# Optimization experiments

Measured on AMD Instinct MI355X. Metric: run time of the kernel, lower is better.

Reference implementation:

```python
import jax, jax.numpy as jnp
import numpy as np

N_NODES = 100000
N_EDGES = 1600000
D_FEAT = 128
UNITS = 128
LEAKY_ALPHA = 0.2  # tf.nn.leaky_relu default


def setup_inputs() -> dict:
    key = jax.random.key(0)
    k1, k2, k3, k4 = jax.random.split(key, 4)
    node_states = jax.random.normal(k1, (N_NODES, D_FEAT), dtype=jnp.float32)
    edges = jax.random.randint(k2, (N_EDGES, 2), 0, N_NODES, dtype=jnp.int64)
    kernel = jax.random.normal(k3, (D_FEAT, UNITS), dtype=jnp.float32) * (1.0 / np.sqrt(D_FEAT))
    kernel_attention = jax.random.normal(k4, (2 * UNITS, 1), dtype=jnp.float32) * (1.0 / np.sqrt(2 * UNITS))
    return {
        "node_states": node_states,
        "edges": edges,
        "kernel": kernel,
        "kernel_attention": kernel_attention,
    }


def reference(node_states, edges, kernel, kernel_attention):
    n = node_states.shape[0]
    tgt_idx = edges[:, 0]
    src_idx = edges[:, 1]

    # node_states_transformed: [N, units]
    h = node_states @ kernel

    # Attention logits. concat([tgt, src]) @ ka == tgt @ ka_t + src @ ka_s
    # (avoids materializing the [E, 2*units] concat).
    ka_t = kernel_attention[:UNITS, 0]   # [units]
    ka_s = kernel_attention[UNITS:, 0]   # [units]
    score_t = h @ ka_t                   # [N]
    score_s = h @ ka_s                   # [N]
    e = score_t[tgt_idx] + score_s[src_idx]              # [E]
    e = jax.nn.leaky_relu(e, negative_slope=LEAKY_ALPHA)
    e = jnp.exp(jnp.clip(e, -2.0, 2.0))

    # Segment softmax over incoming edges of each target node.
    sum_e = jax.ops.segment_sum(e, tgt_idx, num_segments=n)  # [N]
    attention = e / (sum_e[tgt_idx] + 1e-9)                  # [E]

    # Weighted scatter-sum of source messages.
    messages = h[src_idx] * attention[:, None]               # [E, units]
    output = jax.ops.segment_sum(messages, tgt_idx, num_segments=n)  # [N, units]
    return output
```

## Files before the change

### kernel.cpp

```cpp
#include <hip/hip_runtime.h>
#include <stdint.h>

typedef unsigned short ushort_t;
typedef __attribute__((ext_vector_type(8))) short short8;
typedef __attribute__((ext_vector_type(4))) float float4v;
typedef __attribute__((ext_vector_type(2))) float float2v;

#define N_NODES 100000
#define N_EDGES 1600000
#define D 128
#define NB_GEMM 1563
#define NBG     521
#define NB_B1   250
#define EPB     6400
#define BUCKETS 782
#define CAP     2560

static __device__ __forceinline__ float2v up2(uint32_t u) {
    float2v r;
    r.x = __builtin_bit_cast(float, u << 16);
    r.y = __builtin_bit_cast(float, u & 0xffff0000u);
    return r;
}
static __device__ __forceinline__ uint32_t f2bf_u(float f) {
    uint32_t u = __builtin_bit_cast(uint32_t, f);
    return (u + 0x7fffu + ((u >> 16) & 1u)) >> 16;
}
static __device__ __forceinline__ ushort_t f2bf(float f) {
    return (ushort_t)f2bf_u(f);
}
static __device__ __forceinline__ uint32_t pack2(float a, float b) {
    return f2bf_u(a) | (f2bf_u(b) << 16);
}
static __device__ __forceinline__ float edge_e(float s) {
    float x = (s >= 0.0f) ? s : 0.2f * s;
    x = fminf(fmaxf(x, -2.0f), 2.0f);
    return __expf(x);
}

__global__ void __launch_bounds__(256) prep_kernel(const float* __restrict__ W,
                                                   const float* __restrict__ KA,
                                                   float* __restrict__ wa,
                                                   const int* __restrict__ E,
                                                   int* __restrict__ eflag) {
    __shared__ int s;
    int b = blockIdx.x, t = threadIdx.x;
    if (b == 0) {
        if (t == 0) s = 0;
        __syncthreads();
        int nz = 0;
#pragma unroll
        for (int j = 0; j < 8; j++)
            if (E[(t + j * 256) * 2 + 1] != 0) nz = 1;
        if (nz) atomicOr(&s, 1);
        __syncthreads();
        if (t == 0) *eflag = (s == 0) ? 1 : 0;
    } else {
        int half = t >> 7, k = t & 127;
        const float* kav = KA + half * 128;
        const float* wrow = W + k * 128;
        float acc = 0.0f;
#pragma unroll 8
        for (int j = 0; j < 128; j++) acc += wrow[j] * kav[j];
        wa[half * 128 + k] = acc;
    }
}

__global__ void __launch_bounds__(256) fused_kernel(const float* __restrict__ X,
                                                    const float* __restrict__ W,
                                                    const float* __restrict__ wa,
                                                    ushort_t* __restrict__ H,
                                                    float* __restrict__ st,
                                                    float* __restrict__ ss,
                                                    int M,
                                                    const int* __restrict__ E,
                                                    const int* __restrict__ eflag,
                                                    int* __restrict__ sortedE,
                                                    ushort_t* __restrict__ bmat,
                                                    ushort_t* __restrict__ lofs) {
    __shared__ __align__(16) ushort_t lds_raw[16384];
    int tid = threadIdx.x;
    if (blockIdx.x >= NBG) {
        int eb = blockIdx.x - NBG;
        int* lhist = (int*)lds_raw;
        int* lpart = ((int*)lds_raw) + 1024;
        int t = tid;
        for (int j = t; j < 1024; j += 256) lhist[j] = 0;
        __syncthreads();
        int i64 = *eflag;
        int base = eb * EPB;
        int bin[25], w[25];
#pragma unroll
        for (int j = 0; j < 25; j++) {
            int i = base + j * 256 + t;
            int tgt, src;
            if (i64) { uint4 v = *(const uint4*)(E + (size_t)i * 4); tgt = (int)v.x; src = (int)v.z; }
            else     { uint2 v = *(const uint2*)(E + (size_t)i * 2); tgt = (int)v.x; src = (int)v.y; }
            if ((unsigned)tgt >= (unsigned)N_NODES) tgt = 0;
            if ((unsigned)src >= (unsigned)N_NODES) src = 0;
            bin[j] = tgt >> 7;
            w[j]   = ((tgt & 127) << 17) | src;
            atomicAdd(&lhist[bin[j]], 1);
        }
        __syncthreads();
        int c0 = lhist[t * 4], c1 = lhist[t * 4 + 1];
        int c2 = lhist[t * 4 + 2], c3 = lhist[t * 4 + 3];
        int sum = c0 + c1 + c2 + c3;
        lpart[t] = sum;
        __syncthreads();
        for (int off = 1; off < 256; off <<= 1) {
            int x = (t >= off) ? lpart[t - off] : 0;
            __syncthreads();
            lpart[t] += x;
            __syncthreads();
        }
        int e0 = lpart[t] - sum;
        int e1 = e0 + c0, e2 = e1 + c1, e3 = e2 + c2;
        int cc[4] = {c0, c1, c2, c3};
        int ee[4] = {e0, e1, e2, e3};
#pragma unroll
        for (int k = 0; k < 4; k++) {
            int bb = t * 4 + k;
            if (bb < BUCKETS) {
                bmat[eb * BUCKETS + bb] = (ushort_t)cc[k];
                lofs[eb * BUCKETS + bb] = (ushort_t)ee[k];
            }
        }
        lhist[t * 4] = e0; lhist[t * 4 + 1] = e1;
        lhist[t * 4 + 2] = e2; lhist[t * 4 + 3] = e3;
        __syncthreads();
#pragma unroll
        for (int j = 0; j < 25; j++) {
            int pos = atomicAdd(&lhist[bin[j]], 1);
            if (pos < EPB) sortedE[base + pos] = w[j];
        }
        return;
    }
    {
        const float4* W4 = (const float4*)W;
        for (int c = tid; c < 4096; c += 256) {
            float4 w4 = W4[c];
            int i0 = c * 4;
            int k = i0 >> 7;
            int kb = k >> 5, q = (k >> 3) & 3, jj = k & 7;
            const float* wp = (const float*)&w4;
#pragma unroll
            for (int u = 0; u < 4; u++) {
                int nn = (i0 + u) & 127;
                int tt = nn >> 4, l = nn & 15;
                lds_raw[((kb * 8 + tt) * 64 + q * 16 + l) * 8 + jj] = f2bf(wp[u]);
            }
        }
    }
    __syncthreads();

    int wave = tid >> 6, lane = tid & 63;
    int quad = lane >> 4, l16 = lane & 15;
    int t0 = blockIdx.x;

    float4 f[8];
    {
        int ar = t0 * 64 + wave * 16 + l16; if (ar >= M) ar = M - 1;
        const float* xr = X + (size_t)ar * D + quad * 8;
#pragma unroll
        for (int kb = 0; kb < 4; kb++) {
            f[kb * 2]     = *(const float4*)(xr + kb * 32);
            f[kb * 2 + 1] = *(const float4*)(xr + kb * 32 + 4);
        }
    }
#pragma unroll
    for (int it = 0; it < 3; it++) {
        int m0 = (t0 + it * NBG) * 64 + wave * 16;
        float4 nf[8];
        if (it < 2) {
            int ar = (t0 + (it + 1) * NBG) * 64 + wave * 16 + l16;
            if (ar >= M) ar = M - 1;
            const float* xr = X + (size_t)ar * D + quad * 8;
#pragma unroll
            for (int kb = 0; kb < 4; kb++) {
                nf[kb * 2]     = *(const float4*)(xr + kb * 32);
                nf[kb * 2 + 1] = *(const float4*)(xr + kb * 32 + 4);
            }
        }
        short8 a[4];
        float sct = 0.0f, scs = 0.0f;
#pragma unroll
        for (int kb = 0; kb < 4; kb++) {
            float4 f0 = f[kb * 2], f1 = f[kb * 2 + 1];
            const float* wt0 = wa + kb * 32 + quad * 8;
            float4 t0v = *(const float4*)(wt0);
            float4 t1v = *(const float4*)(wt0 + 4);
            float4 s0v = *(const float4*)(wt0 + 128);
            float4 s1v = *(const float4*)(wt0 + 132);
            sct += f0.x * t0v.x + f0.y * t0v.y + f0.z * t0v.z + f0.w * t0v.w
                 + f1.x * t1v.x + f1.y * t1v.y + f1.z * t1v.z + f1.w * t1v.w;
            scs += f0.x * s0v.x + f0.y * s0v.y + f0.z * s0v.z + f0.w * s0v.w
                 + f1.x * s1v.x + f1.y * s1v.y + f1.z * s1v.z + f1.w * s1v.w;
            short8 v;
            v[0] = (short)f2bf(f0.x); v[1] = (short)f2bf(f0.y);
            v[2] = (short)f2bf(f0.z); v[3] = (short)f2bf(f0.w);
            v[4] = (short)f2bf(f1.x); v[5] = (short)f2bf(f1.y);
            v[6] = (short)f2bf(f1.z); v[7] = (short)f2bf(f1.w);
            a[kb] = v;
        }
        sct += __shfl_xor(sct, 16); sct += __shfl_xor(sct, 32);
        scs += __shfl_xor(scs, 16); scs += __shfl_xor(scs, 32);
        if (quad == 0 && m0 + l16 < M) { st[m0 + l16] = sct; ss[m0 + l16] = scs; }

        float4v acc[8] = {};
#pragma unroll
        for (int kb = 0; kb < 4; kb++) {
#pragma unroll
            for (int t = 0; t < 8; t++) {
                short8 b = *(const short8*)(&lds_raw[((kb * 8 + t) * 64 + lane) * 8]);
                acc[t] = __builtin_amdgcn_mfma_f32_16x16x32_bf16(a[kb], b, acc[t], 0, 0, 0);
            }
        }
#pragma unroll
        for (int r = 0; r < 4; r++) {
            int orow = m0 + quad * 4 + r;
            if (orow < M) {
                uint4 v;
                v.x = pack2(acc[0][r], acc[1][r]);
                v.y = pack2(acc[2][r], acc[3][r]);
                v.z = pack2(acc[4][r], acc[5][r]);
                v.w = pack2(acc[6][r], acc[7][r]);
                *(uint4*)(H + (size_t)orow * D + l16 * 8) = v;
            }
        }
        if (it < 2) {
#pragma unroll
            for (int j = 0; j < 8; j++) f[j] = nf[j];
        }
    }
}

__global__ void __launch_bounds__(512) agg2_kernel(const ushort_t* __restrict__ bmat,
                                                   const ushort_t* __restrict__ lofs,
                                                   const int* __restrict__ sortedE,
                                                   const float* __restrict__ st,
                                                   const float* __restrict__ ss,
                                                   const ushort_t* __restrict__ H,
                                                   float* __restrict__ out) {
    __shared__ int stage[CAP];
    __shared__ int sortedLoc[CAP];
    __shared__ int lh[128];
    __shared__ int lrp[129];
    __shared__ int wsum[8];
    __shared__ int lsoff[NB_B1];
    __shared__ int lsst[NB_B1];
    int b = blockIdx.x, t = threadIdx.x;
    int lane = t & 63, wv = t >> 6;
    int cnt = 0, sst = 0;
    if (t < NB_B1) {
        cnt = bmat[t * BUCKETS + b];
        sst = lofs[t * BUCKETS + b];
    }
    int x = cnt;
#pragma unroll
    for (int off = 1; off < 64; off <<= 1) {
        int y = __shfl_up(x, off);
        if (lane >= off) x += y;
    }
    if (lane == 63) wsum[wv] = x;
    if (t < 128) lh[t] = 0;
    __syncthreads();
    int wbase = 0, total = 0;
#pragma unroll
    for (int w = 0; w < 8; w++) {
        int sv = wsum[w];
        if (w < wv) wbase += sv;
        total += sv;
    }
    if (total > CAP) total = CAP;
    int soff = wbase + x - cnt;
    if (t < NB_B1) { lsoff[t] = soff; lsst[t] = sst; }
    __syncthreads();
    for (int j = t; j < total; j += 512) {
        int lo = 0, hi = NB_B1 - 1;
        while (lo < hi) {
            int mid = (lo + hi + 1) >> 1;
            if (lsoff[mid] <= j) lo = mid; else hi = mid - 1;
        }
        stage[j] = sortedE[lo * EPB + lsst[lo] + (j - lsoff[lo])];
    }
    __syncthreads();
    for (int j = t; j < total; j += 512)
        atomicAdd(&lh[stage[j] >> 17], 1);
    __syncthreads();
    int v = (t < 128) ? lh[t] : 0;
    int xs = v;
#pragma unroll
    for (int off = 1; off < 64; off <<= 1) {
        int y = __shfl_up(xs, off);
        if (lane >= off) xs += y;
    }
    if (t == 63) wsum[0] = xs;
    __syncthreads();
    if (t < 128) {
        int inc = (wv == 1) ? xs + wsum[0] : xs;
        int ex = inc - v;
        lrp[t] = ex;
        lh[t]  = ex;
    }
    if (t == 0) lrp[128] = total;
    __syncthreads();
    for (int j = t; j < total; j += 512) {
        int p = stage[j];
        int pos = atomicAdd(&lh[p >> 17], 1);
        if (pos < total) sortedLoc[pos] = p & 0x1FFFF;
    }
    __syncthreads();
    int g = lane >> 4, l = lane & 15;
    for (int nd = wv; nd < 128; nd += 8) {
        int gnode = b * 128 + nd;
        if (gnode >= N_NODES) break;
        int start = lrp[nd], end = lrp[nd + 1];
        float stn = st[gnode];
        float den = 0.0f;
        float2v acc2[4] = {};
        int m = start + g;
        for (; m + 12 < end; m += 16) {
            int s0 = sortedLoc[m],     s1 = sortedLoc[m + 4];
            int s2 = sortedLoc[m + 8], s3 = sortedLoc[m + 12];
            float e0 = edge_e(stn + ss[s0]);
            float e1 = edge_e(stn + ss[s1]);
            float e2 = edge_e(stn + ss[s2]);
            float e3 = edge_e(stn + ss[s3]);
            den += (e0 + e1) + (e2 + e3);
            uint4 p0 = *(const uint4*)(H + ((unsigned)s0 << 7) + l * 8);
            uint4 p1 = *(const uint4*)(H + ((unsigned)s1 << 7) + l * 8);
            uint4 p2 = *(const uint4*)(H + ((unsigned)s2 << 7) + l * 8);
            uint4 p3 = *(const uint4*)(H + ((unsigned)s3 << 7) + l * 8);
            float2v E0 = {e0, e0}, E1 = {e1, e1}, E2 = {e2, e2}, E3 = {e3, e3};
            acc2[0] += E0 * up2(p0.x) + E1 * up2(p1.x) + E2 * up2(p2.x) + E3 * up2(p3.x);
            acc2[1] += E0 * up2(p0.y) + E1 * up2(p1.y) + E2 * up2(p2.y) + E3 * up2(p3.y);
            acc2[2] += E0 * up2(p0.z) + E1 * up2(p1.z) + E2 * up2(p2.z) + E3 * up2(p3.z);
            acc2[3] += E0 * up2(p0.w) + E1 * up2(p1.w) + E2 * up2(p2.w) + E3 * up2(p3.w);
        }
        for (; m + 4 < end; m += 8) {
            int s0 = sortedLoc[m], s1 = sortedLoc[m + 4];
            float e0 = edge_e(stn + ss[s0]);
            float e1 = edge_e(stn + ss[s1]);
            den += e0 + e1;
            uint4 p0 = *(const uint4*)(H + ((unsigned)s0 << 7) + l * 8);
            uint4 p1 = *(const uint4*)(H + ((unsigned)s1 << 7) + l * 8);
            float2v E0 = {e0, e0}, E1 = {e1, e1};
            acc2[0] += E0 * up2(p0.x) + E1 * up2(p1.x);
            acc2[1] += E0 * up2(p0.y) + E1 * up2(p1.y);
            acc2[2] += E0 * up2(p0.z) + E1 * up2(p1.z);
            acc2[3] += E0 * up2(p0.w) + E1 * up2(p1.w);
        }
        if (m < end) {
            int s0 = sortedLoc[m];
            float e0 = edge_e(stn + ss[s0]);
            den += e0;
            uint4 p0 = *(const uint4*)(H + ((unsigned)s0 << 7) + l * 8);
            float2v E0 = {e0, e0};
            acc2[0] += E0 * up2(p0.x);
            acc2[1] += E0 * up2(p0.y);
            acc2[2] += E0 * up2(p0.z);
            acc2[3] += E0 * up2(p0.w);
        }
        den += __shfl_xor(den, 16);
        den += __shfl_xor(den, 32);
        float r[8];
#pragma unroll
        for (int j = 0; j < 4; j++) {
            float a0 = acc2[j].x, a1 = acc2[j].y;
            a0 += __shfl_xor(a0, 16); a0 += __shfl_xor(a0, 32);
            a1 += __shfl_xor(a1, 16); a1 += __shfl_xor(a1, 32);
            r[j * 2] = a0; r[j * 2 + 1] = a1;
        }
        float inv = 1.0f / (den + 1e-9f);
        if (g == 0) {
#pragma unroll
            for (int k = 0; k < 8; k++)
                out[(size_t)gnode * D + k * 16 + l] = r[k] * inv;
        }
    }
}

extern "C" void kernel_launch(void* const* d_in, const int* in_sizes, int n_in,
                              void* d_out, int out_size, void* d_ws, size_t ws_size,
                              hipStream_t stream) {
    const float* X  = (const float*)d_in[0];
    const int*   E  = (const int*)d_in[1];
    const float* W  = (const float*)d_in[2];
    const float* KA = (const float*)d_in[3];
    for (int i = 0; i < n_in; i++) {
        int s = in_sizes[i];
        if (s == N_NODES * D)      X  = (const float*)d_in[i];
        else if (s == N_EDGES * 2) E  = (const int*)d_in[i];
        else if (s == D * D)       W  = (const float*)d_in[i];
        else if (s == 2 * D)       KA = (const float*)d_in[i];
    }
    float* out = (float*)d_out;

    char* ws = (char*)d_ws;
    ushort_t* H        = (ushort_t*)(ws + 0);
    float*    wa       = (float*)   (ws + 25600000);
    float*    st       = (float*)   (ws + 25601024);
    float*    ssb      = (float*)   (ws + 26001024);
    int*      sortedE  = (int*)     (ws + 26401024);
    ushort_t* bmat     = (ushort_t*)(ws + 32801024);
    ushort_t* lofs     = (ushort_t*)(ws + 33192032);
    int*      eflag    = (int*)     (ws + 33583040);

    prep_kernel<<<2, 256, 0, stream>>>(W, KA, wa, E, eflag);
    fused_kernel<<<NBG + NB_B1, 256, 0, stream>>>(X, W, wa, H, st, ssb,
                                                  N_NODES, E, eflag,
                                                  sortedE, bmat, lofs);
    agg2_kernel<<<BUCKETS, 512, 0, stream>>>(bmat, lofs, sortedE, st, ssb,
                                             H, out);
}
```

Measured before the change: 215.3 us.

## Fold prep kernel into fused kernel and split aggregation buckets across two blocks

```diff
diff --git a/kernel.cpp b/kernel.cpp
--- a/kernel.cpp
+++ b/kernel.cpp
@@ -38,56 +38,36 @@
     return __expf(x);
 }
 
-__global__ void __launch_bounds__(256) prep_kernel(const float* __restrict__ W,
-                                                   const float* __restrict__ KA,
-                                                   float* __restrict__ wa,
-                                                   const int* __restrict__ E,
-                                                   int* __restrict__ eflag) {
-    __shared__ int s;
-    int b = blockIdx.x, t = threadIdx.x;
-    if (b == 0) {
-        if (t == 0) s = 0;
-        __syncthreads();
-        int nz = 0;
-#pragma unroll
-        for (int j = 0; j < 8; j++)
-            if (E[(t + j * 256) * 2 + 1] != 0) nz = 1;
-        if (nz) atomicOr(&s, 1);
-        __syncthreads();
-        if (t == 0) *eflag = (s == 0) ? 1 : 0;
-    } else {
-        int half = t >> 7, k = t & 127;
-        const float* kav = KA + half * 128;
-        const float* wrow = W + k * 128;
-        float acc = 0.0f;
-#pragma unroll 8
-        for (int j = 0; j < 128; j++) acc += wrow[j] * kav[j];
-        wa[half * 128 + k] = acc;
-    }
-}
-
 __global__ void __launch_bounds__(256) fused_kernel(const float* __restrict__ X,
                                                     const float* __restrict__ W,
-                                                    const float* __restrict__ wa,
+                                                    const float* __restrict__ KA,
                                                     ushort_t* __restrict__ H,
                                                     float* __restrict__ st,
                                                     float* __restrict__ ss,
                                                     int M,
                                                     const int* __restrict__ E,
-                                                    const int* __restrict__ eflag,
                                                     int* __restrict__ sortedE,
                                                     ushort_t* __restrict__ bmat,
                                                     ushort_t* __restrict__ lofs) {
     __shared__ __align__(16) ushort_t lds_raw[16384];
+    __shared__ float lds_wa[256];
+    __shared__ int   ldet;
     int tid = threadIdx.x;
     if (blockIdx.x >= NBG) {
         int eb = blockIdx.x - NBG;
         int* lhist = (int*)lds_raw;
         int* lpart = ((int*)lds_raw) + 1024;
         int t = tid;
+        if (t == 0) ldet = 0;
         for (int j = t; j < 1024; j += 256) lhist[j] = 0;
         __syncthreads();
-        int i64 = *eflag;
+        int nz = 0;
+#pragma unroll
+        for (int j = 0; j < 8; j++)
+            if (E[(t + j * 256) * 2 + 1] != 0) nz = 1;
+        if (nz) atomicOr(&ldet, 1);
+        __syncthreads();
+        int i64 = (ldet == 0) ? 1 : 0;
         int base = eb * EPB;
         int bin[25], w[25];
 #pragma unroll
@@ -151,6 +131,13 @@
                 lds_raw[((kb * 8 + tt) * 64 + q * 16 + l) * 8 + jj] = f2bf(wp[u]);
             }
         }
+        int half = tid >> 7, k = tid & 127;
+        const float* kav = KA + half * 128;
+        const float* wrow = W + k * 128;
+        float acc = 0.0f;
+#pragma unroll 8
+        for (int j = 0; j < 128; j++) acc += wrow[j] * kav[j];
+        lds_wa[half * 128 + k] = acc;
     }
     __syncthreads();
 
@@ -187,7 +174,7 @@
 #pragma unroll
         for (int kb = 0; kb < 4; kb++) {
             float4 f0 = f[kb * 2], f1 = f[kb * 2 + 1];
-            const float* wt0 = wa + kb * 32 + quad * 8;
+            const float* wt0 = lds_wa + kb * 32 + quad * 8;
             float4 t0v = *(const float4*)(wt0);
             float4 t1v = *(const float4*)(wt0 + 4);
             float4 s0v = *(const float4*)(wt0 + 128);
@@ -249,7 +236,8 @@
     __shared__ int wsum[8];
     __shared__ int lsoff[NB_B1];
     __shared__ int lsst[NB_B1];
-    int b = blockIdx.x, t = threadIdx.x;
+    int b = blockIdx.x >> 1, half = blockIdx.x & 1;
+    int t = threadIdx.x;
     int lane = t & 63, wv = t >> 6;
     int cnt = 0, sst = 0;
     if (t < NB_B1) {
@@ -312,7 +300,8 @@
     }
     __syncthreads();
     int g = lane >> 4, l = lane & 15;
-    for (int nd = wv; nd < 128; nd += 8) {
+    for (int nd0 = wv; nd0 < 64; nd0 += 8) {
+        int nd = half * 64 + nd0;
         int gnode = b * 128 + nd;
         if (gnode >= N_NODES) break;
         int start = lrp[nd], end = lrp[nd + 1];
@@ -399,18 +388,15 @@
 
     char* ws = (char*)d_ws;
     ushort_t* H        = (ushort_t*)(ws + 0);
-    float*    wa       = (float*)   (ws + 25600000);
     float*    st       = (float*)   (ws + 25601024);
     float*    ssb      = (float*)   (ws + 26001024);
     int*      sortedE  = (int*)     (ws + 26401024);
     ushort_t* bmat     = (ushort_t*)(ws + 32801024);
     ushort_t* lofs     = (ushort_t*)(ws + 33192032);
-    int*      eflag    = (int*)     (ws + 33583040);
-
-    prep_kernel<<<2, 256, 0, stream>>>(W, KA, wa, E, eflag);
-    fused_kernel<<<NBG + NB_B1, 256, 0, stream>>>(X, W, wa, H, st, ssb,
-                                                  N_NODES, E, eflag,
+
+    fused_kernel<<<NBG + NB_B1, 256, 0, stream>>>(X, W, KA, H, st, ssb,
+                                                  N_NODES, E,
                                                   sortedE, bmat, lofs);
-    agg2_kernel<<<BUCKETS, 512, 0, stream>>>(bmat, lofs, sortedE, st, ssb,
-                                             H, out);
-}
+    agg2_kernel<<<2 * BUCKETS, 512, 0, stream>>>(bmat, lofs, sortedE, st, ssb,
+                                                 H, out);
+}
```

Result: no change. 214.9 us (-0.2%).
